# Kernel tuning notes

Hardware: AMD Instinct MI355X
Metric: run time of the kernel (lower is better)

## Reference

```python
import jax, jax.numpy as jnp
import numpy as np
from jax import lax
from jax.scipy.special import logsumexp

B, T, H, L = 64, 512, 768, 9


def setup_inputs() -> dict:
    key = jax.random.key(0)
    k1, k2, k3, k4, k5 = jax.random.split(key, 5)
    hidden = jax.random.normal(k1, (B, T, H), dtype=jnp.float32)
    W = jax.random.normal(k2, (L, H), dtype=jnp.float32) * 0.02
    b = jnp.zeros((L,), dtype=jnp.float32)
    transitions = jax.random.normal(k3, (L, L), dtype=jnp.float32) * 0.1
    lengths = jax.random.randint(k4, (B,), T // 2, T + 1)
    seq_mask = jnp.arange(T)[None, :] < lengths[:, None]          # [B,T] bool
    labels = jax.random.randint(k5, (B, T), 0, L).astype(jnp.int32)
    labels = jnp.where(seq_mask, labels, -100).astype(jnp.int32)   # -100 = ignore
    attention_mask = seq_mask.astype(jnp.int32)
    return {"hidden": hidden, "W": W, "b": b, "transitions": transitions,
            "labels": labels, "attention_mask": attention_mask}


def _crf_nll(logits, tags, transitions, mask):
    # numerator: joint score of the gold path (no start/end transitions)
    maskf = mask.astype(logits.dtype)
    emit = jnp.take_along_axis(logits, tags[..., None], axis=2)[..., 0]   # [B,T]
    emit_score = (emit * maskf).sum(-1)
    trans = transitions[tags[:, :-1], tags[:, 1:]]                        # [B,T-1]
    trans_score = (trans * maskf[:, 1:]).sum(-1)
    numerator = emit_score + trans_score
    # denominator: forward algorithm (log-sum-exp recurrence over time)
    def step(alpha, xs):
        logit_t, mask_t = xs                                   # [B,L], [B]
        inner = alpha[:, :, None] + transitions[None, :, :] + logit_t[:, None, :]
        new = logsumexp(inner, axis=1)
        return jnp.where(mask_t[:, None], new, alpha), None
    alpha0 = logits[:, 0]                                      # mask[:,0] assumed True
    alpha, _ = lax.scan(step, alpha0,
                        (jnp.transpose(logits[:, 1:], (1, 0, 2)), mask[:, 1:].T))
    denominator = logsumexp(alpha, axis=-1)
    return -(numerator - denominator).sum()


def _viterbi(logits, transitions, mask):
    num_tags = transitions.shape[0]
    identity_bp = jnp.broadcast_to(jnp.arange(num_tags)[None, :], logits.shape[:1] + (num_tags,))

    def vstep(vscore, xs):
        logit_t, mask_t = xs
        inner = vscore[:, :, None] + transitions[None, :, :]   # [B,L_prev,L_cur]
        bp = jnp.argmax(inner, axis=1)                         # [B,L]
        new = jnp.max(inner, axis=1) + logit_t
        vscore = jnp.where(mask_t[:, None], new, vscore)
        bp = jnp.where(mask_t[:, None], bp, identity_bp)       # carry tag through pad
        return vscore, bp

    vscore0 = logits[:, 0]
    vscore, bps = lax.scan(vstep, vscore0,
                           (jnp.transpose(logits[:, 1:], (1, 0, 2)), mask[:, 1:].T))
    last_tag = jnp.argmax(vscore, axis=-1)                     # [B]

    def btstep(tag, bp_t):
        prev = jnp.take_along_axis(bp_t, tag[:, None], axis=1)[:, 0]
        return prev, tag

    first_tag, tags_rest = lax.scan(btstep, last_tag, bps, reverse=True)  # ys[t]=tag_{t+1}
    return jnp.concatenate([first_tag[:, None], tags_rest.T], axis=1)     # [B,T]


def reference(hidden, W, b, transitions, labels, attention_mask):
    mask = (attention_mask != 0) & (labels != -100)            # create_combined_mask
    logits = jnp.einsum('bth,lh->btl', hidden, W) + b          # classifier (dropout=eval)
    tags = jnp.where(labels == -100, 0, labels)                # adjust_labels_for_crf
    loss = _crf_nll(logits, tags, transitions, mask)           # -log_likelihood (summed)
    vtags = _viterbi(logits, transitions, mask)                # [B,T]
    # pad_predictions: prepend -100, shift right, -100 outside the masked span
    bsz = hidden.shape[0]
    neg = jnp.full((bsz, 1), -100, dtype=jnp.int32)
    shifted = jnp.concatenate([neg, vtags[:, :-1].astype(jnp.int32)], axis=1)
    valid = jnp.concatenate([jnp.zeros((bsz, 1), bool), mask[:, :-1]], axis=1)
    predictions = jnp.where(valid, shifted, -100)
    return loss, predictions
```

## Files before the change

### kernel.cpp

```cpp
#include <hip/hip_runtime.h>

#define BATCH 64
#define TLEN  512
#define HDIM  768
#define LTAGS 9

#define WS_LOGD 0
#define WS_LOGF 2359296
#define WS_VM   3538944
#define WS_AM   6193152
#define WS_NUM  6856704
#define WS_LOSS 6857216

__global__ __launch_bounds__(256) void logits_kernel(
    const float* __restrict__ hidden, const float* __restrict__ W,
    const float* __restrict__ bvec, double* __restrict__ logitsD,
    float* __restrict__ logitsF)
{
    __shared__ float sW[LTAGS * HDIM];
    __shared__ float sb[LTAGS];
    const int tid = threadIdx.x;
    for (int i = tid; i < LTAGS * HDIM; i += 256) sW[i] = W[i];
    if (tid < LTAGS) sb[tid] = bvec[tid];
    __syncthreads();

    const int lane = tid & 63;
    const int wave = tid >> 6;
    const int sub  = lane & 7;
    const int rg   = lane >> 3;

    const int rowBase = blockIdx.x * 64 + wave * 16;
    const int r0 = rowBase + rg;
    const int r1 = rowBase + rg + 8;
    const float* h0p = hidden + (size_t)r0 * HDIM;
    const float* h1p = hidden + (size_t)r1 * HDIM;

    double acc0[LTAGS], acc1[LTAGS];
    #pragma unroll
    for (int l = 0; l < LTAGS; ++l) { acc0[l] = 0.0; acc1[l] = 0.0; }

    #pragma unroll 2
    for (int i = 0; i < 24; ++i) {
        const int off = i * 32 + sub * 4;
        const float4 h0 = *(const float4*)(h0p + off);
        const float4 h1 = *(const float4*)(h1p + off);
        #pragma unroll
        for (int l = 0; l < LTAGS; ++l) {
            const float4 w = *(const float4*)&sW[l * HDIM + off];
            float d0 = h0.x * w.x;
            d0 = fmaf(h0.y, w.y, d0); d0 = fmaf(h0.z, w.z, d0); d0 = fmaf(h0.w, w.w, d0);
            float d1 = h1.x * w.x;
            d1 = fmaf(h1.y, w.y, d1); d1 = fmaf(h1.z, w.z, d1); d1 = fmaf(h1.w, w.w, d1);
            acc0[l] += (double)d0;
            acc1[l] += (double)d1;
        }
    }
    #pragma unroll
    for (int l = 0; l < LTAGS; ++l) {
        double v0 = acc0[l], v1 = acc1[l];
        #pragma unroll
        for (int off = 4; off > 0; off >>= 1) {
            v0 += __shfl_down(v0, off);
            v1 += __shfl_down(v1, off);
        }
        acc0[l] = v0; acc1[l] = v1;
    }
    if (sub == 0) {
        #pragma unroll
        for (int l = 0; l < LTAGS; ++l) {
            double v0 = acc0[l] + (double)sb[l];
            double v1 = acc1[l] + (double)sb[l];
            logitsD[(size_t)r0 * LTAGS + l] = v0;
            logitsD[(size_t)r1 * LTAGS + l] = v1;
            logitsF[(size_t)r0 * LTAGS + l] = (float)v0;
            logitsF[(size_t)r1 * LTAGS + l] = (float)v1;
        }
    }
}

__global__ __launch_bounds__(256) void chunk_kernel(
    const float* __restrict__ trans, const int* __restrict__ labels,
    const int* __restrict__ att, const double* __restrict__ logitsD,
    const float* __restrict__ logitsF,
    double* __restrict__ wsVM, float* __restrict__ wsAM,
    double* __restrict__ wsNum)
{
    __shared__ double sT64[81];
    __shared__ float  sE32[81];
    const int tid = threadIdx.x;
    if (tid < 81) { float tv = trans[tid]; sT64[tid] = (double)tv; sE32[tid] = __expf(tv); }
    __syncthreads();

    const int blk = blockIdx.x;
    if (blk < 144) {
        const int gid = blk * 256 + tid;
        const int b   = gid / 576;
        const int rem = gid - b * 576;
        const int c   = rem / 9;
        const int i   = rem - c * 9;

        double M[LTAGS];
        #pragma unroll
        for (int j = 0; j < LTAGS; ++j) M[j] = (i == j) ? 0.0 : -1e300;

        const double* lrow = logitsD + ((size_t)b * TLEN + (c * 8 + 1)) * LTAGS;
        const int* lab = labels + b * TLEN;
        const int* am  = att + b * TLEN;
        const int t0 = c * 8 + 1;

        double lg[LTAGS], lgN[LTAGS];
        #pragma unroll
        for (int j = 0; j < LTAGS; ++j) lg[j] = lrow[j];
        bool mk = (am[t0] != 0) && (lab[t0] != -100);

        for (int s = 0; s < 8; ++s) {
            bool mkN = false;
            const int tn = t0 + s + 1;
            if (s < 7 && tn <= TLEN - 1) {
                const double* ln = lrow + (s + 1) * LTAGS;
                #pragma unroll
                for (int j = 0; j < LTAGS; ++j) lgN[j] = ln[j];
                mkN = (am[tn] != 0) && (lab[tn] != -100);
            }
            double nw[LTAGS];
            #pragma unroll
            for (int j = 0; j < LTAGS; ++j) {
                double bst = M[0] + sT64[j];
                #pragma unroll
                for (int k = 1; k < LTAGS; ++k) {
                    double cnd = M[k] + sT64[k * LTAGS + j];
                    bst = fmax(bst, cnd);
                }
                nw[j] = bst + lg[j];
            }
            #pragma unroll
            for (int j = 0; j < LTAGS; ++j) { M[j] = mk ? nw[j] : M[j]; lg[j] = lgN[j]; }
            mk = mkN;
        }
        double* dst = wsVM + (((size_t)b * 64 + c) * LTAGS + i) * LTAGS;
        #pragma unroll
        for (int j = 0; j < LTAGS; ++j) dst[j] = M[j];
    } else if (blk < 216) {
        const int gid = (blk - 144) * 256 + tid;
        const int b   = gid / 288;
        const int rem = gid - b * 288;
        const int c   = rem / 9;
        const int i   = rem - c * 9;

        float M[LTAGS];
        #pragma unroll
        for (int j = 0; j < LTAGS; ++j) M[j] = (i == j) ? 0.f : -1e30f;

        const float* lrow = logitsF + ((size_t)b * TLEN + (c * 16 + 1)) * LTAGS;
        const int* lab = labels + b * TLEN;
        const int* am  = att + b * TLEN;
        const int t0 = c * 16 + 1;

        float lg[LTAGS], lgN[LTAGS];
        #pragma unroll
        for (int j = 0; j < LTAGS; ++j) lg[j] = lrow[j];
        bool mk = (am[t0] != 0) && (lab[t0] != -100);

        for (int s = 0; s < 16; ++s) {
            bool mkN = false;
            const int tn = t0 + s + 1;
            if (s < 15 && tn <= TLEN - 1) {
                const float* ln = lrow + (s + 1) * LTAGS;
                #pragma unroll
                for (int j = 0; j < LTAGS; ++j) lgN[j] = ln[j];
                mkN = (am[tn] != 0) && (lab[tn] != -100);
            }
            float m = M[0];
            #pragma unroll
            for (int k = 1; k < LTAGS; ++k) m = fmaxf(m, M[k]);
            float P[LTAGS];
            #pragma unroll
            for (int k = 0; k < LTAGS; ++k) P[k] = __expf(M[k] - m);
            float nw[LTAGS];
            #pragma unroll
            for (int j = 0; j < LTAGS; ++j) {
                float sacc = P[0] * sE32[j];
                #pragma unroll
                for (int k = 1; k < LTAGS; ++k) sacc = fmaf(P[k], sE32[k * LTAGS + j], sacc);
                nw[j] = m + __logf(sacc) + lg[j];
            }
            #pragma unroll
            for (int j = 0; j < LTAGS; ++j) { M[j] = mk ? nw[j] : M[j]; lg[j] = lgN[j]; }
            mk = mkN;
        }
        float* dst = wsAM + (((size_t)b * 32 + c) * LTAGS + i) * LTAGS;
        #pragma unroll
        for (int j = 0; j < LTAGS; ++j) dst[j] = M[j];
    } else {
        const int bb   = (blk - 216) * 4 + (tid >> 6);
        const int lane = tid & 63;
        const int* lab = labels + bb * TLEN;
        const int* am  = att + bb * TLEN;
        const double* lrowb = logitsD + (size_t)bb * TLEN * LTAGS;
        double part = 0.0;
        #pragma unroll
        for (int k = 0; k < 8; ++k) {
            const int t = lane + k * 64;
            int lv = lab[t], av = am[t];
            bool mkc = (av != 0) && (lv != -100);
            int tg = (lv == -100) ? 0 : lv;
            if (mkc) part += lrowb[(size_t)t * LTAGS + tg];
            if (t < TLEN - 1) {
                int lv2 = lab[t + 1], av2 = am[t + 1];
                bool mk2 = (av2 != 0) && (lv2 != -100);
                int tg2 = (lv2 == -100) ? 0 : lv2;
                if (mk2) part += sT64[tg * LTAGS + tg2];
            }
        }
        #pragma unroll
        for (int off = 32; off > 0; off >>= 1) part += __shfl_down(part, off);
        if (lane == 0) wsNum[bb] = part;
    }
}

__global__ __launch_bounds__(128) void crf2_kernel(
    const float* __restrict__ trans, const int* __restrict__ labels,
    const int* __restrict__ att, const double* __restrict__ logitsD,
    const double* __restrict__ wsVM, const float* __restrict__ wsAM,
    const double* __restrict__ wsNum, double* __restrict__ wsLoss,
    float* __restrict__ out)
{
    __shared__ __align__(16) double sVM[64 * 81];
    __shared__ __align__(16) float  sAM[32 * 81];
    __shared__ double sVstart[65 * LTAGS];
    __shared__ unsigned long long sBPp[513];
    __shared__ int sTagB[65];
    __shared__ double sT64[81];
    __shared__ unsigned char sMk[513];
    __shared__ double sDen;
    __shared__ int sLast;

    const int b = blockIdx.x, tid = threadIdx.x;
    const int wave = tid >> 6, lane = tid & 63;
    const unsigned long long IDMAP = 0x876543210ull;

    const double2* gVM = (const double2*)(wsVM + (size_t)b * 64 * 81);
    double2* sVM2 = (double2*)sVM;
    for (int i = tid; i < 2592; i += 128) sVM2[i] = gVM[i];
    const float4* gAM = (const float4*)(wsAM + (size_t)b * 32 * 81);
    float4* sAM4 = (float4*)sAM;
    for (int i = tid; i < 648; i += 128) sAM4[i] = gAM[i];

    const int* lab = labels + b * TLEN;
    const int* am  = att + b * TLEN;
    for (int t = tid; t < TLEN; t += 128) {
        int lv = lab[t], av = am[t];
        sMk[t] = (av != 0 && lv != -100) ? 1 : 0;
    }
    if (tid == 0) sMk[TLEN] = 0;
    if (tid < 81) sT64[tid] = (double)trans[tid];
    __syncthreads();

    if (wave == 0) {
        const int j = (lane < LTAGS) ? lane : (LTAGS - 1);
        double v = logitsD[(size_t)b * TLEN * LTAGS + j];
        double Mc[LTAGS], Mn[LTAGS];
        #pragma unroll
        for (int i = 0; i < LTAGS; ++i) Mc[i] = sVM[i * LTAGS + j];
        for (int c = 0; c < 64; ++c) {
            if (c < 63) {
                #pragma unroll
                for (int i = 0; i < LTAGS; ++i) Mn[i] = sVM[(c + 1) * 81 + i * LTAGS + j];
            }
            if (lane < LTAGS) sVstart[c * LTAGS + j] = v;
            double g[LTAGS];
            #pragma unroll
            for (int i = 0; i < LTAGS; ++i) g[i] = __shfl(v, i);
            double bst = g[0] + Mc[0];
            #pragma unroll
            for (int i = 1; i < LTAGS; ++i) bst = fmax(bst, g[i] + Mc[i]);
            v = bst;
            if (c < 63) {
                #pragma unroll
                for (int i = 0; i < LTAGS; ++i) Mc[i] = Mn[i];
            }
        }
        if (lane < LTAGS) sVstart[64 * LTAGS + j] = v;
        double g[LTAGS];
        #pragma unroll
        for (int i = 0; i < LTAGS; ++i) g[i] = __shfl(v, i);
        if (lane == 0) {
            int bi = 0; double bv = g[0];
            #pragma unroll
            for (int i = 1; i < LTAGS; ++i) if (g[i] > bv) { bv = g[i]; bi = i; }
            sLast = bi;
        }
    } else {
        const int j = (lane < LTAGS) ? lane : (LTAGS - 1);
        float v = (float)logitsD[(size_t)b * TLEN * LTAGS + j];
        float Mc[LTAGS], Mn[LTAGS];
        #pragma unroll
        for (int i = 0; i < LTAGS; ++i) Mc[i] = sAM[i * LTAGS + j];
        for (int c = 0; c < 32; ++c) {
            if (c < 31) {
                #pragma unroll
                for (int i = 0; i < LTAGS; ++i) Mn[i] = sAM[(c + 1) * 81 + i * LTAGS + j];
            }
            float g[LTAGS];
            #pragma unroll
            for (int i = 0; i < LTAGS; ++i) g[i] = __shfl(v, i);
            float a[LTAGS];
            #pragma unroll
            for (int i = 0; i < LTAGS; ++i) a[i] = g[i] + Mc[i];
            float m = a[0];
            #pragma unroll
            for (int i = 1; i < LTAGS; ++i) m = fmaxf(m, a[i]);
            float sacc = 0.f;
            #pragma unroll
            for (int i = 0; i < LTAGS; ++i) sacc += __expf(a[i] - m);
            v = m + __logf(sacc);
            if (c < 31) {
                #pragma unroll
                for (int i = 0; i < LTAGS; ++i) Mc[i] = Mn[i];
            }
        }
        float g[LTAGS];
        #pragma unroll
        for (int i = 0; i < LTAGS; ++i) g[i] = __shfl(v, i);
        if (lane == 0) {
            float m = g[0];
            #pragma unroll
            for (int i = 1; i < LTAGS; ++i) m = fmaxf(m, g[i]);
            float sacc = 0.f;
            #pragma unroll
            for (int i = 0; i < LTAGS; ++i) sacc += __expf(g[i] - m);
            sDen = (double)(m + __logf(sacc));
        }
    }
    __syncthreads();

    unsigned long long S = IDMAP;
    if (tid < 64) {
        const int c = tid;
        double v[LTAGS];
        #pragma unroll
        for (int j = 0; j < LTAGS; ++j) v[j] = sVstart[c * LTAGS + j];
        const double* lrow = logitsD + ((size_t)b * TLEN + (c * 8 + 1)) * LTAGS;
        double lg[LTAGS], lgN[LTAGS];
        #pragma unroll
        for (int j = 0; j < LTAGS; ++j) lg[j] = lrow[j];

        for (int s = 0; s < 8; ++s) {
            const int t = c * 8 + 1 + s;
            if (s < 7 && t + 1 <= TLEN - 1) {
                const double* ln = lrow + (s + 1) * LTAGS;
                #pragma unroll
                for (int j = 0; j < LTAGS; ++j) lgN[j] = ln[j];
            }
            const bool mk = (sMk[t] != 0);
            unsigned long long pk = 0;
            double nv[LTAGS];
            #pragma unroll
            for (int j = 0; j < LTAGS; ++j) {
                double bst = v[0] + sT64[j];
                int bi = 0;
                #pragma unroll
                for (int k = 1; k < LTAGS; ++k) {
                    double cnd = v[k] + sT64[k * LTAGS + j];
                    bool gt = cnd > bst;
                    bst = gt ? cnd : bst;
                    bi  = gt ? k : bi;
                }
                nv[j] = bst + lg[j];
                pk |= ((unsigned long long)bi) << (4 * j);
            }
            pk = mk ? pk : IDMAP;
            sBPp[t] = pk;
            #pragma unroll
            for (int j = 0; j < LTAGS; ++j) { v[j] = mk ? nv[j] : v[j]; lg[j] = lgN[j]; }
        }
        unsigned long long G = IDMAP;
        for (int s = 7; s >= 0; --s) {
            const unsigned long long bp = sBPp[c * 8 + 1 + s];
            unsigned long long ng = 0;
            #pragma unroll
            for (int j = 0; j < LTAGS; ++j) {
                int gj = (int)((G >> (4 * j)) & 15);
                int f  = (int)((bp >> (4 * gj)) & 15);
                ng |= ((unsigned long long)f) << (4 * j);
            }
            G = ng;
        }
        S = G;
    }

    #pragma unroll
    for (int d = 1; d < 64; d <<= 1) {
        unsigned long long Sn = __shfl_down(S, d);
        if (wave == 0 && lane + d < 64) {
            unsigned long long R = 0;
            #pragma unroll
            for (int x = 0; x < LTAGS; ++x) {
                int y = (int)((Sn >> (4 * x)) & 15);
                int z = (int)((S >> (4 * y)) & 15);
                R |= ((unsigned long long)z) << (4 * x);
            }
            S = R;
        }
    }
    if (tid < 64) {
        const int lt = sLast;
        sTagB[tid] = (int)((S >> (4 * lt)) & 15);
        if (tid == 0) sTagB[64] = lt;
    }
    __syncthreads();

    if (tid < 64) {
        const int c = tid;
        int cur = sTagB[c + 1];
        float* po = out + 1 + b * TLEN;
        for (int s = 8; s >= 1; --s) {
            const int t = c * 8 + s;
            if (t < TLEN) {
                int nxt = (int)((sBPp[t] >> (4 * cur)) & 15);
                po[t] = sMk[t - 1] ? (float)nxt : -100.f;
                cur = nxt;
            }
        }
    }
    if (tid == 0) {
        out[1 + b * TLEN] = -100.f;
        wsLoss[b] = sDen - wsNum[b];
    }
}

__global__ __launch_bounds__(64) void loss_kernel(
    const double* __restrict__ wsLoss, float* __restrict__ out)
{
    double v = wsLoss[threadIdx.x];
    #pragma unroll
    for (int off = 32; off > 0; off >>= 1) v += __shfl_down(v, off);
    if (threadIdx.x == 0) out[0] = (float)v;
}

extern "C" void kernel_launch(void* const* d_in, const int* in_sizes, int n_in,
                              void* d_out, int out_size, void* d_ws, size_t ws_size,
                              hipStream_t stream)
{
    const float* hidden = (const float*)d_in[0];
    const float* W      = (const float*)d_in[1];
    const float* bvec   = (const float*)d_in[2];
    const float* trans  = (const float*)d_in[3];
    const int*   labels = (const int*)d_in[4];
    const int*   att    = (const int*)d_in[5];
    float* out = (float*)d_out;

    char* ws = (char*)d_ws;
    double* logitsD = (double*)(ws + WS_LOGD);
    float*  logitsF = (float*)(ws + WS_LOGF);
    double* wsVM    = (double*)(ws + WS_VM);
    float*  wsAM    = (float*)(ws + WS_AM);
    double* wsNum   = (double*)(ws + WS_NUM);
    double* wsLoss  = (double*)(ws + WS_LOSS);

    logits_kernel<<<512, 256, 0, stream>>>(hidden, W, bvec, logitsD, logitsF);
    chunk_kernel<<<232, 256, 0, stream>>>(trans, labels, att, logitsD, logitsF,
                                          wsVM, wsAM, wsNum);
    crf2_kernel<<<BATCH, 128, 0, stream>>>(trans, labels, att, logitsD,
                                           wsVM, wsAM, wsNum, wsLoss, out);
    loss_kernel<<<1, 64, 0, stream>>>(wsLoss, out);
}
```

Measured before the change: 217.9 us.

## Drop float logits copy, vectorize transition reads, fold loss reduction into atomics

Removes the separate float32 logits buffer, so the forward chunk pass reads the double logits and converts them on load. Transition matrices in shared memory are padded to row strides of 10 and 12 so rows can be read with vector loads, and the max/sum loops are reordered to stream over the source tag. Max reductions are turned into trees. The final loss kernel is eliminated: chunk_kernel zeroes the output and each batch block atomically adds its loss. This saves one launch, but float atomics make the summation order nondeterministic.

New measurement: 219.2 us. Within noise of the previous version (+0.6%).

```diff
diff --git a/kernel.cpp b/kernel.cpp
--- a/kernel.cpp
+++ b/kernel.cpp
@@ -6,16 +6,13 @@
 #define LTAGS 9
 
 #define WS_LOGD 0
-#define WS_LOGF 2359296
-#define WS_VM   3538944
-#define WS_AM   6193152
-#define WS_NUM  6856704
-#define WS_LOSS 6857216
+#define WS_VM   2359296
+#define WS_AM   5013504
+#define WS_NUM  5677056
 
 __global__ __launch_bounds__(256) void logits_kernel(
     const float* __restrict__ hidden, const float* __restrict__ W,
-    const float* __restrict__ bvec, double* __restrict__ logitsD,
-    float* __restrict__ logitsF)
+    const float* __restrict__ bvec, double* __restrict__ logitsD)
 {
     __shared__ float sW[LTAGS * HDIM];
     __shared__ float sb[LTAGS];
@@ -68,12 +65,8 @@
     if (sub == 0) {
         #pragma unroll
         for (int l = 0; l < LTAGS; ++l) {
-            double v0 = acc0[l] + (double)sb[l];
-            double v1 = acc1[l] + (double)sb[l];
-            logitsD[(size_t)r0 * LTAGS + l] = v0;
-            logitsD[(size_t)r1 * LTAGS + l] = v1;
-            logitsF[(size_t)r0 * LTAGS + l] = (float)v0;
-            logitsF[(size_t)r1 * LTAGS + l] = (float)v1;
+            logitsD[(size_t)r0 * LTAGS + l] = acc0[l] + (double)sb[l];
+            logitsD[(size_t)r1 * LTAGS + l] = acc1[l] + (double)sb[l];
         }
     }
 }
@@ -81,14 +74,19 @@
 __global__ __launch_bounds__(256) void chunk_kernel(
     const float* __restrict__ trans, const int* __restrict__ labels,
     const int* __restrict__ att, const double* __restrict__ logitsD,
-    const float* __restrict__ logitsF,
     double* __restrict__ wsVM, float* __restrict__ wsAM,
-    double* __restrict__ wsNum)
+    double* __restrict__ wsNum, float* __restrict__ out)
 {
-    __shared__ double sT64[81];
-    __shared__ float  sE32[81];
+    __shared__ __align__(16) double sT64[90];
+    __shared__ __align__(16) float  sE32[108];
     const int tid = threadIdx.x;
-    if (tid < 81) { float tv = trans[tid]; sT64[tid] = (double)tv; sE32[tid] = __expf(tv); }
+    if (tid < 81) {
+        const int k = tid / 9, j = tid - 9 * k;
+        float tv = trans[tid];
+        sT64[k * 10 + j] = (double)tv;
+        sE32[k * 12 + j] = __expf(tv);
+    }
+    if (blockIdx.x == 0 && tid == 0) out[0] = 0.f;
     __syncthreads();
 
     const int blk = blockIdx.x;
@@ -124,17 +122,30 @@
             }
             double nw[LTAGS];
             #pragma unroll
+            for (int k = 0; k < LTAGS; ++k) {
+                const double2* r = (const double2*)&sT64[k * 10];
+                const double2 r01 = r[0], r23 = r[1], r45 = r[2], r67 = r[3];
+                const double r8 = sT64[k * 10 + 8];
+                const double mk64 = M[k];
+                if (k == 0) {
+                    nw[0] = mk64 + r01.x; nw[1] = mk64 + r01.y;
+                    nw[2] = mk64 + r23.x; nw[3] = mk64 + r23.y;
+                    nw[4] = mk64 + r45.x; nw[5] = mk64 + r45.y;
+                    nw[6] = mk64 + r67.x; nw[7] = mk64 + r67.y;
+                    nw[8] = mk64 + r8;
+                } else {
+                    nw[0] = fmax(nw[0], mk64 + r01.x); nw[1] = fmax(nw[1], mk64 + r01.y);
+                    nw[2] = fmax(nw[2], mk64 + r23.x); nw[3] = fmax(nw[3], mk64 + r23.y);
+                    nw[4] = fmax(nw[4], mk64 + r45.x); nw[5] = fmax(nw[5], mk64 + r45.y);
+                    nw[6] = fmax(nw[6], mk64 + r67.x); nw[7] = fmax(nw[7], mk64 + r67.y);
+                    nw[8] = fmax(nw[8], mk64 + r8);
+                }
+            }
+            #pragma unroll
             for (int j = 0; j < LTAGS; ++j) {
-                double bst = M[0] + sT64[j];
-                #pragma unroll
-                for (int k = 1; k < LTAGS; ++k) {
-                    double cnd = M[k] + sT64[k * LTAGS + j];
-                    bst = fmax(bst, cnd);
-                }
-                nw[j] = bst + lg[j];
-            }
-            #pragma unroll
-            for (int j = 0; j < LTAGS; ++j) { M[j] = mk ? nw[j] : M[j]; lg[j] = lgN[j]; }
+                M[j] = mk ? (nw[j] + lg[j]) : M[j];
+                lg[j] = lgN[j];
+            }
             mk = mkN;
         }
         double* dst = wsVM + (((size_t)b * 64 + c) * LTAGS + i) * LTAGS;
@@ -151,23 +162,23 @@
         #pragma unroll
         for (int j = 0; j < LTAGS; ++j) M[j] = (i == j) ? 0.f : -1e30f;
 
-        const float* lrow = logitsF + ((size_t)b * TLEN + (c * 16 + 1)) * LTAGS;
+        const double* lrow = logitsD + ((size_t)b * TLEN + (c * 16 + 1)) * LTAGS;
         const int* lab = labels + b * TLEN;
         const int* am  = att + b * TLEN;
         const int t0 = c * 16 + 1;
 
         float lg[LTAGS], lgN[LTAGS];
         #pragma unroll
-        for (int j = 0; j < LTAGS; ++j) lg[j] = lrow[j];
+        for (int j = 0; j < LTAGS; ++j) lg[j] = (float)lrow[j];
         bool mk = (am[t0] != 0) && (lab[t0] != -100);
 
         for (int s = 0; s < 16; ++s) {
             bool mkN = false;
             const int tn = t0 + s + 1;
             if (s < 15 && tn <= TLEN - 1) {
-                const float* ln = lrow + (s + 1) * LTAGS;
-                #pragma unroll
-                for (int j = 0; j < LTAGS; ++j) lgN[j] = ln[j];
+                const double* ln = lrow + (s + 1) * LTAGS;
+                #pragma unroll
+                for (int j = 0; j < LTAGS; ++j) lgN[j] = (float)ln[j];
                 mkN = (am[tn] != 0) && (lab[tn] != -100);
             }
             float m = M[0];
@@ -176,16 +187,31 @@
             float P[LTAGS];
             #pragma unroll
             for (int k = 0; k < LTAGS; ++k) P[k] = __expf(M[k] - m);
-            float nw[LTAGS];
+            float sa[LTAGS];
+            #pragma unroll
+            for (int k = 0; k < LTAGS; ++k) {
+                const float4* r = (const float4*)&sE32[k * 12];
+                const float4 f03 = r[0], f47 = r[1];
+                const float f8 = sE32[k * 12 + 8];
+                const float pk = P[k];
+                if (k == 0) {
+                    sa[0] = pk * f03.x; sa[1] = pk * f03.y; sa[2] = pk * f03.z; sa[3] = pk * f03.w;
+                    sa[4] = pk * f47.x; sa[5] = pk * f47.y; sa[6] = pk * f47.z; sa[7] = pk * f47.w;
+                    sa[8] = pk * f8;
+                } else {
+                    sa[0] = fmaf(pk, f03.x, sa[0]); sa[1] = fmaf(pk, f03.y, sa[1]);
+                    sa[2] = fmaf(pk, f03.z, sa[2]); sa[3] = fmaf(pk, f03.w, sa[3]);
+                    sa[4] = fmaf(pk, f47.x, sa[4]); sa[5] = fmaf(pk, f47.y, sa[5]);
+                    sa[6] = fmaf(pk, f47.z, sa[6]); sa[7] = fmaf(pk, f47.w, sa[7]);
+                    sa[8] = fmaf(pk, f8,    sa[8]);
+                }
+            }
             #pragma unroll
             for (int j = 0; j < LTAGS; ++j) {
-                float sacc = P[0] * sE32[j];
-                #pragma unroll
-                for (int k = 1; k < LTAGS; ++k) sacc = fmaf(P[k], sE32[k * LTAGS + j], sacc);
-                nw[j] = m + __logf(sacc) + lg[j];
-            }
-            #pragma unroll
-            for (int j = 0; j < LTAGS; ++j) { M[j] = mk ? nw[j] : M[j]; lg[j] = lgN[j]; }
+                float nwj = m + __logf(sa[j]) + lg[j];
+                M[j] = mk ? nwj : M[j];
+                lg[j] = lgN[j];
+            }
             mk = mkN;
         }
         float* dst = wsAM + (((size_t)b * 32 + c) * LTAGS + i) * LTAGS;
@@ -209,7 +235,7 @@
                 int lv2 = lab[t + 1], av2 = am[t + 1];
                 bool mk2 = (av2 != 0) && (lv2 != -100);
                 int tg2 = (lv2 == -100) ? 0 : lv2;
-                if (mk2) part += sT64[tg * LTAGS + tg2];
+                if (mk2) part += sT64[tg * 10 + tg2];
             }
         }
         #pragma unroll
@@ -222,15 +248,14 @@
     const float* __restrict__ trans, const int* __restrict__ labels,
     const int* __restrict__ att, const double* __restrict__ logitsD,
     const double* __restrict__ wsVM, const float* __restrict__ wsAM,
-    const double* __restrict__ wsNum, double* __restrict__ wsLoss,
-    float* __restrict__ out)
+    const double* __restrict__ wsNum, float* __restrict__ out)
 {
     __shared__ __align__(16) double sVM[64 * 81];
     __shared__ __align__(16) float  sAM[32 * 81];
     __shared__ double sVstart[65 * LTAGS];
     __shared__ unsigned long long sBPp[513];
     __shared__ int sTagB[65];
-    __shared__ double sT64[81];
+    __shared__ __align__(16) double sT64[90];
     __shared__ unsigned char sMk[513];
     __shared__ double sDen;
     __shared__ int sLast;
@@ -253,7 +278,10 @@
         sMk[t] = (av != 0 && lv != -100) ? 1 : 0;
     }
     if (tid == 0) sMk[TLEN] = 0;
-    if (tid < 81) sT64[tid] = (double)trans[tid];
+    if (tid < 81) {
+        const int k = tid / 9, j = tid - 9 * k;
+        sT64[k * 10 + j] = (double)trans[tid];
+    }
     __syncthreads();
 
     if (wave == 0) {
@@ -271,10 +299,12 @@
             double g[LTAGS];
             #pragma unroll
             for (int i = 0; i < LTAGS; ++i) g[i] = __shfl(v, i);
-            double bst = g[0] + Mc[0];
-            #pragma unroll
-            for (int i = 1; i < LTAGS; ++i) bst = fmax(bst, g[i] + Mc[i]);
-            v = bst;
+            double a0 = g[0] + Mc[0], a1 = g[1] + Mc[1], a2 = g[2] + Mc[2];
+            double a3 = g[3] + Mc[3], a4 = g[4] + Mc[4], a5 = g[5] + Mc[5];
+            double a6 = g[6] + Mc[6], a7 = g[7] + Mc[7], a8 = g[8] + Mc[8];
+            double t01 = fmax(a0, a1), t23 = fmax(a2, a3);
+            double t45 = fmax(a4, a5), t67 = fmax(a6, a7);
+            v = fmax(fmax(fmax(t01, t23), fmax(t45, t67)), a8);
             if (c < 63) {
                 #pragma unroll
                 for (int i = 0; i < LTAGS; ++i) Mc[i] = Mn[i];
@@ -307,9 +337,9 @@
             float a[LTAGS];
             #pragma unroll
             for (int i = 0; i < LTAGS; ++i) a[i] = g[i] + Mc[i];
-            float m = a[0];
-            #pragma unroll
-            for (int i = 1; i < LTAGS; ++i) m = fmaxf(m, a[i]);
+            float t01 = fmaxf(a[0], a[1]), t23 = fmaxf(a[2], a[3]);
+            float t45 = fmaxf(a[4], a[5]), t67 = fmaxf(a[6], a[7]);
+            float m = fmaxf(fmaxf(fmaxf(t01, t23), fmaxf(t45, t67)), a[8]);
             float sacc = 0.f;
             #pragma unroll
             for (int i = 0; i < LTAGS; ++i) sacc += __expf(a[i] - m);
@@ -353,26 +383,43 @@
                 for (int j = 0; j < LTAGS; ++j) lgN[j] = ln[j];
             }
             const bool mk = (sMk[t] != 0);
+            double bst[LTAGS];
+            int bi[LTAGS];
+            #pragma unroll
+            for (int k = 0; k < LTAGS; ++k) {
+                const double2* r = (const double2*)&sT64[k * 10];
+                const double2 r01 = r[0], r23 = r[1], r45 = r[2], r67 = r[3];
+                const double r8 = sT64[k * 10 + 8];
+                const double vk = v[k];
+                double cnd[LTAGS];
+                cnd[0] = vk + r01.x; cnd[1] = vk + r01.y;
+                cnd[2] = vk + r23.x; cnd[3] = vk + r23.y;
+                cnd[4] = vk + r45.x; cnd[5] = vk + r45.y;
+                cnd[6] = vk + r67.x; cnd[7] = vk + r67.y;
+                cnd[8] = vk + r8;
+                if (k == 0) {
+                    #pragma unroll
+                    for (int j = 0; j < LTAGS; ++j) { bst[j] = cnd[j]; bi[j] = 0; }
+                } else {
+                    #pragma unroll
+                    for (int j = 0; j < LTAGS; ++j) {
+                        bool gt = cnd[j] > bst[j];
+                        bst[j] = gt ? cnd[j] : bst[j];
+                        bi[j]  = gt ? k : bi[j];
+                    }
+                }
+            }
             unsigned long long pk = 0;
-            double nv[LTAGS];
-            #pragma unroll
-            for (int j = 0; j < LTAGS; ++j) {
-                double bst = v[0] + sT64[j];
-                int bi = 0;
-                #pragma unroll
-                for (int k = 1; k < LTAGS; ++k) {
-                    double cnd = v[k] + sT64[k * LTAGS + j];
-                    bool gt = cnd > bst;
-                    bst = gt ? cnd : bst;
-                    bi  = gt ? k : bi;
-                }
-                nv[j] = bst + lg[j];
-                pk |= ((unsigned long long)bi) << (4 * j);
-            }
+            #pragma unroll
+            for (int j = 0; j < LTAGS; ++j)
+                pk |= ((unsigned long long)bi[j]) << (4 * j);
             pk = mk ? pk : IDMAP;
             sBPp[t] = pk;
             #pragma unroll
-            for (int j = 0; j < LTAGS; ++j) { v[j] = mk ? nv[j] : v[j]; lg[j] = lgN[j]; }
+            for (int j = 0; j < LTAGS; ++j) {
+                v[j] = mk ? (bst[j] + lg[j]) : v[j];
+                lg[j] = lgN[j];
+            }
         }
         unsigned long long G = IDMAP;
         for (int s = 7; s >= 0; --s) {
@@ -425,17 +472,8 @@
     }
     if (tid == 0) {
         out[1 + b * TLEN] = -100.f;
-        wsLoss[b] = sDen - wsNum[b];
-    }
-}
-
-__global__ __launch_bounds__(64) void loss_kernel(
-    const double* __restrict__ wsLoss, float* __restrict__ out)
-{
-    double v = wsLoss[threadIdx.x];
-    #pragma unroll
-    for (int off = 32; off > 0; off >>= 1) v += __shfl_down(v, off);
-    if (threadIdx.x == 0) out[0] = (float)v;
+        atomicAdd(out, (float)(sDen - wsNum[b]));
+    }
 }
 
 extern "C" void kernel_launch(void* const* d_in, const int* in_sizes, int n_in,
@@ -452,16 +490,13 @@
 
     char* ws = (char*)d_ws;
     double* logitsD = (double*)(ws + WS_LOGD);
-    float*  logitsF = (float*)(ws + WS_LOGF);
     double* wsVM    = (double*)(ws + WS_VM);
     float*  wsAM    = (float*)(ws + WS_AM);
     double* wsNum   = (double*)(ws + WS_NUM);
-    double* wsLoss  = (double*)(ws + WS_LOSS);
-
-    logits_kernel<<<512, 256, 0, stream>>>(hidden, W, bvec, logitsD, logitsF);
-    chunk_kernel<<<232, 256, 0, stream>>>(trans, labels, att, logitsD, logitsF,
-                                          wsVM, wsAM, wsNum);
+
+    logits_kernel<<<512, 256, 0, stream>>>(hidden, W, bvec, logitsD);
+    chunk_kernel<<<232, 256, 0, stream>>>(trans, labels, att, logitsD,
+                                          wsVM, wsAM, wsNum, out);
     crf2_kernel<<<BATCH, 128, 0, stream>>>(trans, labels, att, logitsD,
-                                           wsVM, wsAM, wsNum, wsLoss, out);
-    loss_kernel<<<1, 64, 0, stream>>>(wsLoss, out);
+                                           wsVM, wsAM, wsNum, out);
 }
```
